# Kernel tuning notes

Measured on AMD Instinct MI355X. Metric: run time of the kernel, lower is better.

## Reference

```python
import jax, jax.numpy as jnp
import numpy as np

H = 64  # hidden size


def _lstm_layer(x_seq, h0, c0, Wih, Whh, bih, bhh):
    """x_seq: (B,S,I); returns (out (B,S,H), h_final (B,H), c_final (B,H)).
    Gate order matches torch nn.LSTM: i, f, g, o."""
    # Precompute input projections for all timesteps (one big GEMM).
    xproj = jnp.einsum('bsi,gi->bsg', x_seq, Wih) + bih + bhh  # (B,S,4H)

    def step(carry, xp):
        h, c = carry
        gates = xp + h @ Whh.T  # (B,4H)
        i = jax.nn.sigmoid(gates[:, 0 * H:1 * H])
        f = jax.nn.sigmoid(gates[:, 1 * H:2 * H])
        g = jnp.tanh(gates[:, 2 * H:3 * H])
        o = jax.nn.sigmoid(gates[:, 3 * H:4 * H])
        c = f * c + i * g
        h = o * jnp.tanh(c)
        return (h, c), h

    (hT, cT), hs = jax.lax.scan(step, (h0, c0), xproj.transpose(1, 0, 2))
    return hs.transpose(1, 0, 2), hT, cT


def setup_inputs() -> dict:
    key = jax.random.key(0)
    ks = jax.random.split(key, 12)
    B, S, I = 256, 2048, 32
    s_in = 1.0 / np.sqrt(H)
    inp = {
        'x': jax.random.normal(ks[0], (B, S, I), dtype=jnp.float32),
        'h0': jnp.zeros((2, B, H), dtype=jnp.float32),
        'c0': jnp.zeros((2, B, H), dtype=jnp.float32),
        # layer 0 params (torch layout: W_ih (4H,I), W_hh (4H,H))
        'Wih0': jax.random.uniform(ks[1], (4 * H, I), jnp.float32, -s_in, s_in),
        'Whh0': jax.random.uniform(ks[2], (4 * H, H), jnp.float32, -s_in, s_in),
        'bih0': jax.random.uniform(ks[3], (4 * H,), jnp.float32, -s_in, s_in),
        'bhh0': jax.random.uniform(ks[4], (4 * H,), jnp.float32, -s_in, s_in),
        # layer 1 params (input is H)
        'Wih1': jax.random.uniform(ks[5], (4 * H, H), jnp.float32, -s_in, s_in),
        'Whh1': jax.random.uniform(ks[6], (4 * H, H), jnp.float32, -s_in, s_in),
        'bih1': jax.random.uniform(ks[7], (4 * H,), jnp.float32, -s_in, s_in),
        'bhh1': jax.random.uniform(ks[8], (4 * H,), jnp.float32, -s_in, s_in),
        # head
        'Wh': jax.random.uniform(ks[9], (1, H), jnp.float32, -s_in, s_in),
        'bh': jax.random.uniform(ks[10], (1,), jnp.float32, -s_in, s_in),
    }
    return inp


def reference(x, h0, c0, Wih0, Whh0, bih0, bhh0, Wih1, Whh1, bih1, bhh1, Wh, bh):
    # Layer 0
    out0, h_f0, c_f0 = _lstm_layer(x, h0[0], c0[0], Wih0, Whh0, bih0, bhh0)
    # Inter-layer dropout is inactive in eval mode -> identity.
    # Layer 1
    out1, h_f1, c_f1 = _lstm_layer(out0, h0[1], c0[1], Wih1, Whh1, bih1, bhh1)
    probs = jax.nn.sigmoid(out1 @ Wh.T + bh)  # (B,S,1)
    h = jnp.stack([h_f0, h_f1], axis=0)  # (2,B,H)
    c = jnp.stack([c_f0, c_f1], axis=0)
    return probs, h, c
```

## Files before the change

kernel.cpp:

```cpp
#include <hip/hip_runtime.h>
#include <math.h>
#include <stdint.h>

#define SS 2048
#define II 32
#define TB 4

typedef _Float16 f16x8  __attribute__((ext_vector_type(8)));
typedef float    f32x4  __attribute__((ext_vector_type(4)));
typedef uint32_t u32x4e __attribute__((ext_vector_type(4)));
typedef _Float16 f16x2  __attribute__((ext_vector_type(2)));
typedef __fp16   g16x2  __attribute__((ext_vector_type(2)));

union uhc { uint32_t u; f16x2 a; g16x2 b; };
union frag { f16x8 v; uint32_t w[4]; u32x4e q; };

__device__ __forceinline__ uint32_t pk(float x, float y) {
    uhc c; c.b = __builtin_amdgcn_cvt_pkrtz(x, y); return c.u;
}
__device__ __forceinline__ float fdot2(uint32_t a, uint32_t b, float c) {
    uhc x, y; x.u = a; y.u = b;
#if __has_builtin(__builtin_amdgcn_fdot2)
    return __builtin_amdgcn_fdot2(x.a, y.a, c, false);
#else
    return c + (float)x.a.x * (float)y.a.x + (float)x.a.y * (float)y.a.y;
#endif
}
__device__ __forceinline__ float sigm(float x) { return __builtin_amdgcn_rcpf(1.f + __expf(-x)); }
__device__ __forceinline__ float tanh_(float x) {
    x = fminf(fmaxf(x, -15.f), 15.f);
    float e = __expf(-2.f * x);
    return (1.f - e) * __builtin_amdgcn_rcpf(1.f + e);
}
__device__ __forceinline__ frag load8(const float* p) {
    float4 v0 = ((const float4*)p)[0];
    float4 v1 = ((const float4*)p)[1];
    frag f;
    f.w[0] = pk(v0.x, v0.y); f.w[1] = pk(v0.z, v0.w);
    f.w[2] = pk(v1.x, v1.y); f.w[3] = pk(v1.z, v1.w);
    return f;
}
#define MFMA(A, B, C) __builtin_amdgcn_mfma_f32_16x16x32_f16((A).v, (B).v, (C), 0, 0, 0)
#define EXTR(A) (jhi ? (jlo ? (A)[3] : (A)[2]) : (jlo ? (A)[1] : (A)[0]))

__global__ __launch_bounds__(512, 1) void lstm_mfma(
    const float* __restrict__ x,
    const float* __restrict__ h_in, const float* __restrict__ c_in,
    const float* __restrict__ Wih0, const float* __restrict__ Whh0,
    const float* __restrict__ bih0, const float* __restrict__ bhh0,
    const float* __restrict__ Wih1, const float* __restrict__ Whh1,
    const float* __restrict__ bih1, const float* __restrict__ bhh1,
    const float* __restrict__ Wh, const float* __restrict__ bh,
    float* __restrict__ out)
{
    __shared__ uint32_t hbuf[2][2][128];
    __shared__ uint32_t xsb[2][16][64];
    __shared__ float    pbuf[64][4];

    const int tid = threadIdx.x;
    const int w   = tid >> 6, L = tid & 63;
    const int wl  = w & 3;
    const int g16 = L >> 4, b16 = L & 15;
    const int bb  = b16 & 3, j = b16 >> 2;
    const int isL1 = (w >= 4);
    const int u    = 16 * wl + g16 * 4 + j;
    const int bbase = blockIdx.x * TB;
    const int loff  = isL1 ? 16384 : 0;
    const bool jlo = (j & 1) != 0, jhi = (j & 2) != 0;
    const int hoff = ((u >> 3) * 4 + bb) * 16 + (u & 7) * 2;

    const f32x4 zf4 = {0.f, 0.f, 0.f, 0.f};

    float hst = h_in[loff + (size_t)(bbase + bb) * 64 + u];
    float cst = c_in[loff + (size_t)(bbase + bb) * 64 + u];
    *(__fp16*)((char*)&hbuf[1][isL1][0] + hoff) = (__fp16)hst;

    if (tid < 256) {
        const int s_ = tid >> 4, g_ = (tid >> 2) & 3, bb_ = tid & 3;
        const float* p_ = x + (size_t)(bbase + bb_) * (SS * II) + (size_t)s_ * II + g_ * 8;
        float4 v0_ = ((const float4*)p_)[0];
        float4 v1_ = ((const float4*)p_)[1];
        u32x4e wv_ = { pk(v0_.x, v0_.y), pk(v0_.z, v0_.w), pk(v1_.x, v1_.y), pk(v1_.z, v1_.w) };
        *(u32x4e*)((char*)&xsb[0][s_][0] + (g_ * 4 + bb_) * 16) = wv_;
    }
    __syncthreads();

    if (!isL1) {
        frag aH[4][2], aX[4];
        f32x4 bias4[4];
        #pragma unroll
        for (int t = 0; t < 4; ++t) {
            const int arow = t * 64 + 16 * wl + b16;
            aH[t][0] = load8(Whh0 + arow * 64 + g16 * 8);
            aH[t][1] = load8(Whh0 + arow * 64 + 32 + g16 * 8);
            aX[t]    = load8(Wih0 + arow * 32 + g16 * 8);
            const int brow = t * 64 + 16 * wl + g16 * 4;
            float4 q1 = *(const float4*)(bih0 + brow);
            float4 q2 = *(const float4*)(bhh0 + brow);
            bias4[t] = (f32x4){q1.x + q2.x, q1.y + q2.y, q1.z + q2.z, q1.w + q2.w};
        }
        frag whA = load8(Wh + g16 * 8);
        frag whB = load8(Wh + 32 + g16 * 8);
        const float bhs = bh[0];

        float4 xr0, xr1;
        const int s_ = tid >> 4, g_ = (tid >> 2) & 3, bb_ = tid & 3;
        const float* xsrc_base = x + (size_t)(bbase + bb_) * (SS * II) + (size_t)s_ * II + g_ * 8;

        #pragma unroll 2
        for (int it = 0; it <= SS + 1; ++it) {
            if ((it & 15) == 0 && it + 16 < SS) {
                const float* p_ = xsrc_base + (size_t)(((it >> 4) + 1) * 16) * II;
                xr0 = ((const float4*)p_)[0];
                xr1 = ((const float4*)p_)[1];
            }
            if (it < SS) {
                const char* hb = (const char*)&hbuf[(it + 1) & 1][0][0];
                frag bh0, bh1, bx;
                bh0.v = *(const f16x8*)(hb + (g16 * 4 + bb) * 16);
                bh1.v = *(const f16x8*)(hb + ((4 + g16) * 4 + bb) * 16);
                bx.v  = *(const f16x8*)((const char*)&xsb[(it >> 4) & 1][it & 15][0]
                                        + (g16 * 4 + bb) * 16);
                f32x4 p0 = bias4[0], p1 = bias4[1], p2 = bias4[2], p3 = bias4[3];
                p0 = MFMA(aH[0][0], bh0, p0); p1 = MFMA(aH[1][0], bh0, p1);
                p2 = MFMA(aH[2][0], bh0, p2); p3 = MFMA(aH[3][0], bh0, p3);
                p0 = MFMA(aX[0], bx, p0);     p1 = MFMA(aX[1], bx, p1);
                p2 = MFMA(aX[2], bx, p2);     p3 = MFMA(aX[3], bx, p3);
                f32x4 q0 = MFMA(aH[0][1], bh1, zf4), q1 = MFMA(aH[1][1], bh1, zf4);
                f32x4 q2 = MFMA(aH[2][1], bh1, zf4), q3 = MFMA(aH[3][1], bh1, zf4);
                f32x4 a0 = p0 + q0, a1 = p1 + q1, a2 = p2 + q2, a3 = p3 + q3;
                float gi = sigm(EXTR(a0)), gf = sigm(EXTR(a1));
                float gg = tanh_(EXTR(a2)), go = sigm(EXTR(a3));
                cst = gf * cst + gi * gg;
                hst = go * tanh_(cst);
                *(__fp16*)((char*)&hbuf[it & 1][0][0] + hoff) = (__fp16)hst;
            }
            if (w == 0 && it >= 2) {
                const char* h1b = (const char*)&hbuf[it & 1][1][0];
                frag b1, b1k;
                b1.v  = *(const f16x8*)(h1b + (g16 * 4 + bb) * 16);
                b1k.v = *(const f16x8*)(h1b + ((4 + g16) * 4 + bb) * 16);
                float pv = 0.f;
                #pragma unroll
                for (int i = 0; i < 4; ++i) {
                    pv = fdot2(whA.w[i], b1.w[i], pv);
                    pv = fdot2(whB.w[i], b1k.w[i], pv);
                }
                pv += __shfl_xor(pv, 16);
                pv += __shfl_xor(pv, 32);
                pv = sigm(pv + bhs);
                const int t = it - 2;
                if (L < 4) pbuf[t & 63][L] = pv;
                if ((t & 63) == 63) {
                    const int tbase = t & ~63;
                    const int fb = L >> 4, fs = (L & 15) * 4;
                    float4 vv = make_float4(pbuf[fs][fb], pbuf[fs + 1][fb],
                                            pbuf[fs + 2][fb], pbuf[fs + 3][fb]);
                    *(float4*)(out + (size_t)(bbase + fb) * SS + tbase + fs) = vv;
                }
            }
            if ((it & 15) == 8 && it + 8 < SS) {
                const int cn = (it >> 4) + 1;
                u32x4e wv_ = { pk(xr0.x, xr0.y), pk(xr0.z, xr0.w),
                               pk(xr1.x, xr1.y), pk(xr1.z, xr1.w) };
                *(u32x4e*)((char*)&xsb[cn & 1][s_][0] + (g_ * 4 + bb_) * 16) = wv_;
            }
            __syncthreads();
        }
    } else {
        frag aI[4][2], aR[4][2];
        f32x4 bias4[4];
        #pragma unroll
        for (int t = 0; t < 4; ++t) {
            const int arow = t * 64 + 16 * wl + b16;
            aI[t][0] = load8(Wih1 + arow * 64 + g16 * 8);
            aI[t][1] = load8(Wih1 + arow * 64 + 32 + g16 * 8);
            aR[t][0] = load8(Whh1 + arow * 64 + g16 * 8);
            aR[t][1] = load8(Whh1 + arow * 64 + 32 + g16 * 8);
            const int brow = t * 64 + 16 * wl + g16 * 4;
            float4 q1 = *(const float4*)(bih1 + brow);
            float4 q2 = *(const float4*)(bhh1 + brow);
            bias4[t] = (f32x4){q1.x + q2.x, q1.y + q2.y, q1.z + q2.z, q1.w + q2.w};
        }

        #pragma unroll 2
        for (int it = 0; it <= SS + 1; ++it) {
            if (it >= 1 && it <= SS) {
                const char* h1b = (const char*)&hbuf[it & 1][1][0];
                const char* h0b = (const char*)&hbuf[(it + 1) & 1][0][0];
                frag b0, b0k, b1, b1k;
                b0.v  = *(const f16x8*)(h0b + (g16 * 4 + bb) * 16);
                b0k.v = *(const f16x8*)(h0b + ((4 + g16) * 4 + bb) * 16);
                b1.v  = *(const f16x8*)(h1b + (g16 * 4 + bb) * 16);
                b1k.v = *(const f16x8*)(h1b + ((4 + g16) * 4 + bb) * 16);
                f32x4 p0 = bias4[0], p1 = bias4[1], p2 = bias4[2], p3 = bias4[3];
                p0 = MFMA(aI[0][0], b0, p0);  p1 = MFMA(aI[1][0], b0, p1);
                p2 = MFMA(aI[2][0], b0, p2);  p3 = MFMA(aI[3][0], b0, p3);
                p0 = MFMA(aR[0][0], b1, p0);  p1 = MFMA(aR[1][0], b1, p1);
                p2 = MFMA(aR[2][0], b1, p2);  p3 = MFMA(aR[3][0], b1, p3);
                f32x4 q0 = MFMA(aI[0][1], b0k, zf4), q1 = MFMA(aI[1][1], b0k, zf4);
                f32x4 q2 = MFMA(aI[2][1], b0k, zf4), q3 = MFMA(aI[3][1], b0k, zf4);
                q0 = MFMA(aR[0][1], b1k, q0); q1 = MFMA(aR[1][1], b1k, q1);
                q2 = MFMA(aR[2][1], b1k, q2); q3 = MFMA(aR[3][1], b1k, q3);
                f32x4 a0 = p0 + q0, a1 = p1 + q1, a2 = p2 + q2, a3 = p3 + q3;
                float gi = sigm(EXTR(a0)), gf = sigm(EXTR(a1));
                float gg = tanh_(EXTR(a2)), go = sigm(EXTR(a3));
                cst = gf * cst + gi * gg;
                hst = go * tanh_(cst);
                *(__fp16*)((char*)&hbuf[(it + 1) & 1][1][0] + hoff) = (__fp16)hst;
            }
            __syncthreads();
        }
    }

    out[524288 + loff + (size_t)(bbase + bb) * 64 + u] = hst;
    out[557056 + loff + (size_t)(bbase + bb) * 64 + u] = cst;
}

extern "C" void kernel_launch(void* const* d_in, const int* in_sizes, int n_in,
                              void* d_out, int out_size, void* d_ws, size_t ws_size,
                              hipStream_t stream) {
    const float* x    = (const float*)d_in[0];
    const float* h0   = (const float*)d_in[1];
    const float* c0   = (const float*)d_in[2];
    const float* Wih0 = (const float*)d_in[3];
    const float* Whh0 = (const float*)d_in[4];
    const float* bih0 = (const float*)d_in[5];
    const float* bhh0 = (const float*)d_in[6];
    const float* Wih1 = (const float*)d_in[7];
    const float* Whh1 = (const float*)d_in[8];
    const float* bih1 = (const float*)d_in[9];
    const float* bhh1 = (const float*)d_in[10];
    const float* Wh   = (const float*)d_in[11];
    const float* bh   = (const float*)d_in[12];
    float* out = (float*)d_out;

    hipLaunchKernelGGL(lstm_mfma, dim3(256 / TB), dim3(512), 0, stream,
                       x, h0, c0, Wih0, Whh0, bih0, bhh0,
                       Wih1, Whh1, bih1, bhh1, Wh, bh, out);
}
```

Baseline: 1.203 ms.

## Halve batch per block and remap work to 4 waves with 2 MFMA tiles each

Cuts the batch tile per block from 4 to 2, which doubles the grid to 128 blocks, and shrinks each block from 8 waves to 4 (2 per layer). Each wave now computes two 16-row MFMA tiles per gate instead of one, and the gate bias is added in scalar form after the MFMAs instead of seeding the accumulators. The aim is to spread the sequential recurrence across more CUs (the MI355X has 256) and make each per-step __syncthreads cheaper with fewer waves. In exchange each wave issues twice the MFMAs per step on its serial critical path, holds more weight registers, and half of each MFMA's 16 batch columns go unused.

```diff
diff --git a/kernel.cpp b/kernel.cpp
--- a/kernel.cpp
+++ b/kernel.cpp
@@ -4,7 +4,7 @@
 
 #define SS 2048
 #define II 32
-#define TB 4
+#define TB 2
 
 typedef _Float16 f16x8  __attribute__((ext_vector_type(8)));
 typedef float    f32x4  __attribute__((ext_vector_type(4)));
@@ -41,9 +41,10 @@
     return f;
 }
 #define MFMA(A, B, C) __builtin_amdgcn_mfma_f32_16x16x32_f16((A).v, (B).v, (C), 0, 0, 0)
-#define EXTR(A) (jhi ? (jlo ? (A)[3] : (A)[2]) : (jlo ? (A)[1] : (A)[0]))
-
-__global__ __launch_bounds__(512, 1) void lstm_mfma(
+#define EXTR1(A) (jhi ? (jlo ? (A)[3] : (A)[2]) : (jlo ? (A)[1] : (A)[0]))
+#define EXTR(A0, A1) (khi ? EXTR1(A1) : EXTR1(A0))
+
+__global__ __launch_bounds__(256, 1) void lstm_mfma(
     const float* __restrict__ x,
     const float* __restrict__ h_in, const float* __restrict__ c_in,
     const float* __restrict__ Wih0, const float* __restrict__ Whh0,
@@ -53,21 +54,21 @@
     const float* __restrict__ Wh, const float* __restrict__ bh,
     float* __restrict__ out)
 {
-    __shared__ uint32_t hbuf[2][2][128];
-    __shared__ uint32_t xsb[2][16][64];
-    __shared__ float    pbuf[64][4];
+    __shared__ uint32_t hbuf[2][2][64];
+    __shared__ uint32_t xsb[2][16][32];
+    __shared__ float    pbuf[64][2];
 
     const int tid = threadIdx.x;
     const int w   = tid >> 6, L = tid & 63;
-    const int wl  = w & 3;
+    const int q   = w & 1;
+    const int isL1 = (w >= 2);
     const int g16 = L >> 4, b16 = L & 15;
-    const int bb  = b16 & 3, j = b16 >> 2;
-    const int isL1 = (w >= 4);
-    const int u    = 16 * wl + g16 * 4 + j;
+    const int bb  = b16 & 1, j = b16 >> 1;
+    const int u   = 32 * q + 16 * (j >> 2) + 4 * g16 + (j & 3);
     const int bbase = blockIdx.x * TB;
     const int loff  = isL1 ? 16384 : 0;
-    const bool jlo = (j & 1) != 0, jhi = (j & 2) != 0;
-    const int hoff = ((u >> 3) * 4 + bb) * 16 + (u & 7) * 2;
+    const bool jlo = (j & 1) != 0, jhi = (j & 2) != 0, khi = (j & 4) != 0;
+    const int hoff = ((u >> 3) * 2 + bb) * 16 + (u & 7) * 2;
 
     const f32x4 zf4 = {0.f, 0.f, 0.f, 0.f};
 
@@ -75,41 +76,49 @@
     float cst = c_in[loff + (size_t)(bbase + bb) * 64 + u];
     *(__fp16*)((char*)&hbuf[1][isL1][0] + hoff) = (__fp16)hst;
 
-    if (tid < 256) {
-        const int s_ = tid >> 4, g_ = (tid >> 2) & 3, bb_ = tid & 3;
-        const float* p_ = x + (size_t)(bbase + bb_) * (SS * II) + (size_t)s_ * II + g_ * 8;
-        float4 v0_ = ((const float4*)p_)[0];
-        float4 v1_ = ((const float4*)p_)[1];
+    float bias0 = bih0[u] + bhh0[u], bias1, bias2, bias3;
+    if (isL1) {
+        bias0 = bih1[u] + bhh1[u];
+        bias1 = bih1[64 + u] + bhh1[64 + u];
+        bias2 = bih1[128 + u] + bhh1[128 + u];
+        bias3 = bih1[192 + u] + bhh1[192 + u];
+    } else {
+        bias1 = bih0[64 + u] + bhh0[64 + u];
+        bias2 = bih0[128 + u] + bhh0[128 + u];
+        bias3 = bih0[192 + u] + bhh0[192 + u];
+    }
+
+    const int s_ = tid >> 3, g_ = (tid >> 1) & 3, bb_ = tid & 1;
+    const float* xsrc_base = x + (size_t)(bbase + bb_) * (SS * II) + (size_t)s_ * II + g_ * 8;
+
+    if (tid < 128) {
+        float4 v0_ = ((const float4*)xsrc_base)[0];
+        float4 v1_ = ((const float4*)xsrc_base)[1];
         u32x4e wv_ = { pk(v0_.x, v0_.y), pk(v0_.z, v0_.w), pk(v1_.x, v1_.y), pk(v1_.z, v1_.w) };
-        *(u32x4e*)((char*)&xsb[0][s_][0] + (g_ * 4 + bb_) * 16) = wv_;
+        *(u32x4e*)((char*)&xsb[0][s_][0] + (g_ * 2 + bb_) * 16) = wv_;
     }
     __syncthreads();
 
     if (!isL1) {
-        frag aH[4][2], aX[4];
-        f32x4 bias4[4];
+        frag aH[4][2][2], aX[4][2];
         #pragma unroll
         for (int t = 0; t < 4; ++t) {
-            const int arow = t * 64 + 16 * wl + b16;
-            aH[t][0] = load8(Whh0 + arow * 64 + g16 * 8);
-            aH[t][1] = load8(Whh0 + arow * 64 + 32 + g16 * 8);
-            aX[t]    = load8(Wih0 + arow * 32 + g16 * 8);
-            const int brow = t * 64 + 16 * wl + g16 * 4;
-            float4 q1 = *(const float4*)(bih0 + brow);
-            float4 q2 = *(const float4*)(bhh0 + brow);
-            bias4[t] = (f32x4){q1.x + q2.x, q1.y + q2.y, q1.z + q2.z, q1.w + q2.w};
+            #pragma unroll
+            for (int k = 0; k < 2; ++k) {
+                const int arow = t * 64 + 32 * q + 16 * k + b16;
+                aH[t][k][0] = load8(Whh0 + arow * 64 + g16 * 8);
+                aH[t][k][1] = load8(Whh0 + arow * 64 + 32 + g16 * 8);
+                aX[t][k]    = load8(Wih0 + arow * 32 + g16 * 8);
+            }
         }
         frag whA = load8(Wh + g16 * 8);
         frag whB = load8(Wh + 32 + g16 * 8);
         const float bhs = bh[0];
-
         float4 xr0, xr1;
-        const int s_ = tid >> 4, g_ = (tid >> 2) & 3, bb_ = tid & 3;
-        const float* xsrc_base = x + (size_t)(bbase + bb_) * (SS * II) + (size_t)s_ * II + g_ * 8;
 
         #pragma unroll 2
         for (int it = 0; it <= SS + 1; ++it) {
-            if ((it & 15) == 0 && it + 16 < SS) {
+            if ((it & 15) == 0 && it + 16 < SS && tid < 128) {
                 const float* p_ = xsrc_base + (size_t)(((it >> 4) + 1) * 16) * II;
                 xr0 = ((const float4*)p_)[0];
                 xr1 = ((const float4*)p_)[1];
@@ -117,20 +126,25 @@
             if (it < SS) {
                 const char* hb = (const char*)&hbuf[(it + 1) & 1][0][0];
                 frag bh0, bh1, bx;
-                bh0.v = *(const f16x8*)(hb + (g16 * 4 + bb) * 16);
-                bh1.v = *(const f16x8*)(hb + ((4 + g16) * 4 + bb) * 16);
+                bh0.v = *(const f16x8*)(hb + (g16 * 2 + bb) * 16);
+                bh1.v = *(const f16x8*)(hb + ((4 + g16) * 2 + bb) * 16);
                 bx.v  = *(const f16x8*)((const char*)&xsb[(it >> 4) & 1][it & 15][0]
-                                        + (g16 * 4 + bb) * 16);
-                f32x4 p0 = bias4[0], p1 = bias4[1], p2 = bias4[2], p3 = bias4[3];
-                p0 = MFMA(aH[0][0], bh0, p0); p1 = MFMA(aH[1][0], bh0, p1);
-                p2 = MFMA(aH[2][0], bh0, p2); p3 = MFMA(aH[3][0], bh0, p3);
-                p0 = MFMA(aX[0], bx, p0);     p1 = MFMA(aX[1], bx, p1);
-                p2 = MFMA(aX[2], bx, p2);     p3 = MFMA(aX[3], bx, p3);
-                f32x4 q0 = MFMA(aH[0][1], bh1, zf4), q1 = MFMA(aH[1][1], bh1, zf4);
-                f32x4 q2 = MFMA(aH[2][1], bh1, zf4), q3 = MFMA(aH[3][1], bh1, zf4);
-                f32x4 a0 = p0 + q0, a1 = p1 + q1, a2 = p2 + q2, a3 = p3 + q3;
-                float gi = sigm(EXTR(a0)), gf = sigm(EXTR(a1));
-                float gg = tanh_(EXTR(a2)), go = sigm(EXTR(a3));
+                                        + (g16 * 2 + bb) * 16);
+                f32x4 acc[4][2];
+                #pragma unroll
+                for (int t = 0; t < 4; ++t) {
+                    #pragma unroll
+                    for (int k = 0; k < 2; ++k) {
+                        f32x4 p = MFMA(aH[t][k][0], bh0, zf4);
+                        p = MFMA(aX[t][k], bx, p);
+                        f32x4 qq = MFMA(aH[t][k][1], bh1, zf4);
+                        acc[t][k] = p + qq;
+                    }
+                }
+                float gi = sigm(EXTR(acc[0][0], acc[0][1]) + bias0);
+                float gf = sigm(EXTR(acc[1][0], acc[1][1]) + bias1);
+                float gg = tanh_(EXTR(acc[2][0], acc[2][1]) + bias2);
+                float go = sigm(EXTR(acc[3][0], acc[3][1]) + bias3);
                 cst = gf * cst + gi * gg;
                 hst = go * tanh_(cst);
                 *(__fp16*)((char*)&hbuf[it & 1][0][0] + hoff) = (__fp16)hst;
@@ -138,8 +152,8 @@
             if (w == 0 && it >= 2) {
                 const char* h1b = (const char*)&hbuf[it & 1][1][0];
                 frag b1, b1k;
-                b1.v  = *(const f16x8*)(h1b + (g16 * 4 + bb) * 16);
-                b1k.v = *(const f16x8*)(h1b + ((4 + g16) * 4 + bb) * 16);
+                b1.v  = *(const f16x8*)(h1b + (g16 * 2 + bb) * 16);
+                b1k.v = *(const f16x8*)(h1b + ((4 + g16) * 2 + bb) * 16);
                 float pv = 0.f;
                 #pragma unroll
                 for (int i = 0; i < 4; ++i) {
@@ -150,37 +164,37 @@
                 pv += __shfl_xor(pv, 32);
                 pv = sigm(pv + bhs);
                 const int t = it - 2;
-                if (L < 4) pbuf[t & 63][L] = pv;
+                if (L < 2) pbuf[t & 63][L] = pv;
                 if ((t & 63) == 63) {
                     const int tbase = t & ~63;
                     const int fb = L >> 4, fs = (L & 15) * 4;
-                    float4 vv = make_float4(pbuf[fs][fb], pbuf[fs + 1][fb],
-                                            pbuf[fs + 2][fb], pbuf[fs + 3][fb]);
-                    *(float4*)(out + (size_t)(bbase + fb) * SS + tbase + fs) = vv;
-                }
-            }
-            if ((it & 15) == 8 && it + 8 < SS) {
+                    if (L < 32) {
+                        float4 vv = make_float4(pbuf[fs][fb], pbuf[fs + 1][fb],
+                                                pbuf[fs + 2][fb], pbuf[fs + 3][fb]);
+                        *(float4*)(out + (size_t)(bbase + fb) * SS + tbase + fs) = vv;
+                    }
+                }
+            }
+            if ((it & 15) == 8 && it + 8 < SS && tid < 128) {
                 const int cn = (it >> 4) + 1;
                 u32x4e wv_ = { pk(xr0.x, xr0.y), pk(xr0.z, xr0.w),
                                pk(xr1.x, xr1.y), pk(xr1.z, xr1.w) };
-                *(u32x4e*)((char*)&xsb[cn & 1][s_][0] + (g_ * 4 + bb_) * 16) = wv_;
+                *(u32x4e*)((char*)&xsb[cn & 1][s_][0] + (g_ * 2 + bb_) * 16) = wv_;
             }
             __syncthreads();
         }
     } else {
-        frag aI[4][2], aR[4][2];
-        f32x4 bias4[4];
+        frag aI[4][2][2], aR[4][2][2];
         #pragma unroll
         for (int t = 0; t < 4; ++t) {
-            const int arow = t * 64 + 16 * wl + b16;
-            aI[t][0] = load8(Wih1 + arow * 64 + g16 * 8);
-            aI[t][1] = load8(Wih1 + arow * 64 + 32 + g16 * 8);
-            aR[t][0] = load8(Whh1 + arow * 64 + g16 * 8);
-            aR[t][1] = load8(Whh1 + arow * 64 + 32 + g16 * 8);
-            const int brow = t * 64 + 16 * wl + g16 * 4;
-            float4 q1 = *(const float4*)(bih1 + brow);
-            float4 q2 = *(const float4*)(bhh1 + brow);
-            bias4[t] = (f32x4){q1.x + q2.x, q1.y + q2.y, q1.z + q2.z, q1.w + q2.w};
+            #pragma unroll
+            for (int k = 0; k < 2; ++k) {
+                const int arow = t * 64 + 32 * q + 16 * k + b16;
+                aI[t][k][0] = load8(Wih1 + arow * 64 + g16 * 8);
+                aI[t][k][1] = load8(Wih1 + arow * 64 + 32 + g16 * 8);
+                aR[t][k][0] = load8(Whh1 + arow * 64 + g16 * 8);
+                aR[t][k][1] = load8(Whh1 + arow * 64 + 32 + g16 * 8);
+            }
         }
 
         #pragma unroll 2
@@ -189,22 +203,26 @@
                 const char* h1b = (const char*)&hbuf[it & 1][1][0];
                 const char* h0b = (const char*)&hbuf[(it + 1) & 1][0][0];
                 frag b0, b0k, b1, b1k;
-                b0.v  = *(const f16x8*)(h0b + (g16 * 4 + bb) * 16);
-                b0k.v = *(const f16x8*)(h0b + ((4 + g16) * 4 + bb) * 16);
-                b1.v  = *(const f16x8*)(h1b + (g16 * 4 + bb) * 16);
-                b1k.v = *(const f16x8*)(h1b + ((4 + g16) * 4 + bb) * 16);
-                f32x4 p0 = bias4[0], p1 = bias4[1], p2 = bias4[2], p3 = bias4[3];
-                p0 = MFMA(aI[0][0], b0, p0);  p1 = MFMA(aI[1][0], b0, p1);
-                p2 = MFMA(aI[2][0], b0, p2);  p3 = MFMA(aI[3][0], b0, p3);
-                p0 = MFMA(aR[0][0], b1, p0);  p1 = MFMA(aR[1][0], b1, p1);
-                p2 = MFMA(aR[2][0], b1, p2);  p3 = MFMA(aR[3][0], b1, p3);
-                f32x4 q0 = MFMA(aI[0][1], b0k, zf4), q1 = MFMA(aI[1][1], b0k, zf4);
-                f32x4 q2 = MFMA(aI[2][1], b0k, zf4), q3 = MFMA(aI[3][1], b0k, zf4);
-                q0 = MFMA(aR[0][1], b1k, q0); q1 = MFMA(aR[1][1], b1k, q1);
-                q2 = MFMA(aR[2][1], b1k, q2); q3 = MFMA(aR[3][1], b1k, q3);
-                f32x4 a0 = p0 + q0, a1 = p1 + q1, a2 = p2 + q2, a3 = p3 + q3;
-                float gi = sigm(EXTR(a0)), gf = sigm(EXTR(a1));
-                float gg = tanh_(EXTR(a2)), go = sigm(EXTR(a3));
+                b0.v  = *(const f16x8*)(h0b + (g16 * 2 + bb) * 16);
+                b0k.v = *(const f16x8*)(h0b + ((4 + g16) * 2 + bb) * 16);
+                b1.v  = *(const f16x8*)(h1b + (g16 * 2 + bb) * 16);
+                b1k.v = *(const f16x8*)(h1b + ((4 + g16) * 2 + bb) * 16);
+                f32x4 acc[4][2];
+                #pragma unroll
+                for (int t = 0; t < 4; ++t) {
+                    #pragma unroll
+                    for (int k = 0; k < 2; ++k) {
+                        f32x4 p = MFMA(aI[t][k][0], b0, zf4);
+                        p = MFMA(aR[t][k][0], b1, p);
+                        f32x4 qq = MFMA(aI[t][k][1], b0k, zf4);
+                        qq = MFMA(aR[t][k][1], b1k, qq);
+                        acc[t][k] = p + qq;
+                    }
+                }
+                float gi = sigm(EXTR(acc[0][0], acc[0][1]) + bias0);
+                float gf = sigm(EXTR(acc[1][0], acc[1][1]) + bias1);
+                float gg = tanh_(EXTR(acc[2][0], acc[2][1]) + bias2);
+                float go = sigm(EXTR(acc[3][0], acc[3][1]) + bias3);
                 cst = gf * cst + gi * gg;
                 hst = go * tanh_(cst);
                 *(__fp16*)((char*)&hbuf[(it + 1) & 1][1][0] + hoff) = (__fp16)hst;
@@ -235,7 +253,7 @@
     const float* bh   = (const float*)d_in[12];
     float* out = (float*)d_out;
 
-    hipLaunchKernelGGL(lstm_mfma, dim3(256 / TB), dim3(512), 0, stream,
+    hipLaunchKernelGGL(lstm_mfma, dim3(256 / TB), dim3(256), 0, stream,
                        x, h0, c0, Wih0, Whh0, bih0, bhh0,
                        Wih1, Whh1, bih1, bhh1, Wh, bh, out);
 }
```

After: 2.030 ms. 68.8% more time.
